# Kernel tuning notes

Hardware: AMD Instinct MI355X
Metric: run time of the kernel (lower is better)

The kernel has to match this reference:

```python
import jax, jax.numpy as jnp
import numpy as np
from jax import lax

B, T, S_ENC = 64, 32, 64
E, H, V = 1024, 1024, 32000


def setup_inputs() -> dict:
    key = jax.random.key(0)
    ks = jax.random.split(key, 12)
    s = 0.02
    return {
        "inputs": jax.random.randint(ks[0], (B, T), 0, V),
        "encoder_outputs": jax.random.normal(ks[1], (B, S_ENC, 2 * H), jnp.float32),
        "h0": jax.random.normal(ks[2], (B, H), jnp.float32) * 0.1,
        "c0": jax.random.normal(ks[3], (B, H), jnp.float32) * 0.1,
        "emb": jax.random.normal(ks[4], (V, E), jnp.float32) * s,
        "W_ih": jax.random.normal(ks[5], (4 * H, E), jnp.float32) * s,
        "W_hh": jax.random.normal(ks[6], (4 * H, H), jnp.float32) * s,
        "b_ih": jnp.zeros((4 * H,), jnp.float32),
        "b_hh": jnp.zeros((4 * H,), jnp.float32),
        "attn_W": jax.random.normal(ks[7], (2 * H, H), jnp.float32) * s,  # Linear(H -> 2H, no bias)
        "comb_W": jax.random.normal(ks[8], (H, 3 * H), jnp.float32) * s,  # Linear(3H -> H)
        "comb_b": jnp.zeros((H,), jnp.float32),
        "out_W": jax.random.normal(ks[9], (V, H), jnp.float32) * s,       # Linear(H -> V)
        "out_b": jnp.zeros((V,), jnp.float32),
    }


def _decode(inputs, encoder_outputs, h0, c0, emb, W_ih, W_hh, b_ih, b_hh,
            attn_W, comb_W, comb_b, out_W, out_b):
    x = emb[inputs]                      # [B, T, E]
    bias = b_ih + b_hh

    def step(carry, x_t):
        h, c = carry                     # [B, H] each
        gates = x_t @ W_ih.T + h @ W_hh.T + bias    # [B, 4H]
        i, f, g, o = jnp.split(gates, 4, axis=-1)   # PyTorch LSTM gate order
        i, f, o = jax.nn.sigmoid(i), jax.nn.sigmoid(f), jax.nn.sigmoid(o)
        c = f * c + i * jnp.tanh(g)
        h = o * jnp.tanh(c)
        # Luong-style attention (faithful to source, incl. softmax over dim=1 of size 1)
        ah = h @ attn_W.T                                        # [B, 2H]
        scores = jnp.einsum('bd,bsd->bs', ah, encoder_outputs)[:, None, :]  # [B,1,S]
        w = jax.nn.softmax(scores, axis=1)                       # size-1 axis -> all ones
        ctx = jnp.einsum('bqs,bsd->bqd', w, encoder_outputs)[:, 0]          # [B, 2H]
        merged = jnp.concatenate([h, ctx], axis=-1)              # [B, 3H]
        out = jnp.tanh(merged @ comb_W.T + comb_b)               # [B, H]
        return (h, c), out

    (h, c), outs = lax.scan(step, (h0, c0), x.transpose(1, 0, 2))
    outputs = outs.transpose(1, 0, 2)                            # [B, T, H]
    logits = outputs @ out_W.T + out_b                           # [B, T, V]
    return logits, h, c


def reference(inputs, encoder_outputs, h0, c0, emb, W_ih, W_hh, b_ih, b_hh,
              attn_W, comb_W, comb_b, out_W, out_b):
    return _decode(inputs, encoder_outputs, h0, c0, emb, W_ih, W_hh, b_ih, b_hh,
                   attn_W, comb_W, comb_b, out_W, out_b)
```

## Files before the change

### kernel.cpp

```cpp
#include <hip/hip_runtime.h>
#include <hip/hip_bf16.h>


typedef unsigned short u16;
typedef unsigned int u32;
typedef short s8v __attribute__((ext_vector_type(8)));
typedef float f4v __attribute__((ext_vector_type(4)));

__device__ __forceinline__ u16 f2bf(float f) {
  unsigned x = __float_as_uint(f);
  return (u16)((x + 0x7fffu + ((x >> 16) & 1u)) >> 16);
}
__device__ __forceinline__ float bf2f(u16 u) {
  return __uint_as_float(((unsigned)u) << 16);
}

__device__ __forceinline__ void gl_lds16(const void* g, void* l) {
  __builtin_amdgcn_global_load_lds(
      (const __attribute__((address_space(1))) u32*)g,
      (__attribute__((address_space(3))) u32*)l, 16, 0, 0);
}

__device__ __forceinline__ int xcd_swz(int bid, int nb) {
  int q8 = nb >> 3, r8 = nb & 7;
  int xcd = bid & 7, idx = bid >> 3;
  return (xcd < r8 ? xcd * (q8 + 1) : r8 * (q8 + 1) + (xcd - r8) * q8) + idx;
}

template <int EPI>
__global__ __launch_bounds__(512, 1) void gemm_p(
    const u16* __restrict__ A, const u16* __restrict__ Bm,
    const float* __restrict__ bias, void* __restrict__ Cp,
    int K, int ldc, int gridM) {
  __shared__ __align__(16) u16 LDS[3 * 24576];

  int swz = xcd_swz((int)blockIdx.x, (int)gridDim.x);
  int mt = swz % gridM, nt = swz / gridM;
  long bm = (long)mt * 128, bn = (long)nt * 256;

  int tid = threadIdx.x;
  int w = tid >> 6, l = tid & 63;
  int wm = w & 1, wn = w >> 1;
  int lr = l & 15, lg = l >> 4;

  int nt_k = K >> 6;

  auto stage = [&](int s, int kt_idx) {
    int kt = kt_idx << 6;
    u16* sa = &LDS[s * 24576];
    u16* sb = &LDS[s * 24576 + 8192];
#pragma unroll
    for (int ch = 0; ch < 2; ++ch) {
      int cb = ch * 512 + w * 64;
      int c = cb + l;
      int row = c >> 3, sp = c & 7;
      gl_lds16(A + (bm + row) * (long)K + kt + ((sp ^ (row & 7)) << 3),
               sa + cb * 8);
    }
#pragma unroll
    for (int ch = 0; ch < 4; ++ch) {
      int cb = ch * 512 + w * 64;
      int c = cb + l;
      int row = c >> 3, sp = c & 7;
      gl_lds16(Bm + (bn + row) * (long)K + kt + ((sp ^ (row & 7)) << 3),
               sb + cb * 8);
    }
  };

  f4v acc[4][4];
#pragma unroll
  for (int i = 0; i < 4; ++i)
#pragma unroll
    for (int j = 0; j < 4; ++j) acc[i][j] = (f4v){0.f, 0.f, 0.f, 0.f};

  stage(0, 0);
  stage(1, 1);
  asm volatile("s_waitcnt vmcnt(6)" ::: "memory");
  __builtin_amdgcn_s_barrier();
  __builtin_amdgcn_sched_barrier(0);

  for (int t = 0; t < nt_k; ++t) {
    if (t + 2 < nt_k) stage((t + 2) % 3, t + 2);
    const u16* sa = &LDS[(t % 3) * 24576];
    const u16* sb = &LDS[(t % 3) * 24576 + 8192];
#pragma unroll
    for (int ks = 0; ks < 2; ++ks) {
      s8v av[4], bv[4];
#pragma unroll
      for (int i = 0; i < 4; ++i) {
        int ra = wm * 64 + i * 16 + lr;
        int pa = (ks * 4 + lg) ^ (ra & 7);
        av[i] = *(const s8v*)((const char*)sa + ra * 128 + pa * 16);
        int rb = wn * 64 + i * 16 + lr;
        int pb = (ks * 4 + lg) ^ (rb & 7);
        bv[i] = *(const s8v*)((const char*)sb + rb * 128 + pb * 16);
      }
      __builtin_amdgcn_s_setprio(1);
#pragma unroll
      for (int mi = 0; mi < 4; ++mi)
#pragma unroll
        for (int ni = 0; ni < 4; ++ni)
          acc[mi][ni] = __builtin_amdgcn_mfma_f32_16x16x32_bf16(
              av[mi], bv[ni], acc[mi][ni], 0, 0, 0);
      __builtin_amdgcn_s_setprio(0);
    }
    if (t + 1 >= nt_k) break;
    if (t + 2 < nt_k) {
      asm volatile("s_waitcnt vmcnt(6)" ::: "memory");
    } else {
      asm volatile("s_waitcnt vmcnt(0)" ::: "memory");
    }
    __builtin_amdgcn_s_barrier();
    __builtin_amdgcn_sched_barrier(0);
  }

#pragma unroll
  for (int mi = 0; mi < 4; ++mi) {
#pragma unroll
    for (int q = 0; q < 4; ++q) {
      long row = bm + wm * 64 + mi * 16 + lg * 4 + q;
#pragma unroll
      for (int ni = 0; ni < 4; ++ni) {
        long col = bn + wn * 64 + ni * 16 + lr;
        float v = acc[mi][ni][q] + bias[col];
        if (EPI == 3)
          ((float*)Cp)[row * (long)ldc + col] = v;
        else
          ((u16*)Cp)[row * (long)ldc + col] = f2bf(v);
      }
    }
  }
}

template <int EPI>
__global__ __launch_bounds__(256, 2) void gemm_bt2(
    const u16* __restrict__ A, const u16* __restrict__ Bm,
    const float* __restrict__ bias, void* __restrict__ Cp,
    int K, int ldc, int gridM) {
  __shared__ __align__(16) u16 As[128 * 64];
  __shared__ __align__(16) u16 Bs[128 * 64];

  int swz = xcd_swz((int)blockIdx.x, (int)gridDim.x);
  int mt = swz % gridM, nt = swz / gridM;
  long bm = (long)mt * 128, bn = (long)nt * 128;

  int tid = threadIdx.x;
  int w = tid >> 6, l = tid & 63;
  int wm = (w & 1) * 64, wn = (w >> 1) * 64;
  int lr = l & 15, lg = l >> 4;

  f4v acc[4][4];
#pragma unroll
  for (int i = 0; i < 4; ++i)
#pragma unroll
    for (int j = 0; j < 4; ++j) acc[i][j] = (f4v){0.f, 0.f, 0.f, 0.f};

  for (int kt = 0; kt < K; kt += 64) {
#pragma unroll
    for (int p = 0; p < 4; ++p) {
      int cb = (p * 4 + w) * 64;
      int c = cb + l;
      int row = c >> 3, ce = (c & 7) * 8;
      gl_lds16(A + (bm + row) * (long)K + kt + ce, &As[cb * 8]);
      gl_lds16(Bm + (bn + row) * (long)K + kt + ce, &Bs[cb * 8]);
    }
    __syncthreads();
#pragma unroll
    for (int ks = 0; ks < 2; ++ks) {
      int kb = ks * 64 + lg * 16;
      s8v av[4], bv[4];
#pragma unroll
      for (int i = 0; i < 4; ++i) {
        av[i] = *(const s8v*)((const char*)&As[0] + (wm + i * 16 + lr) * 128 + kb);
        bv[i] = *(const s8v*)((const char*)&Bs[0] + (wn + i * 16 + lr) * 128 + kb);
      }
#pragma unroll
      for (int mi = 0; mi < 4; ++mi)
#pragma unroll
        for (int ni = 0; ni < 4; ++ni)
          acc[mi][ni] = __builtin_amdgcn_mfma_f32_16x16x32_bf16(
              av[mi], bv[ni], acc[mi][ni], 0, 0, 0);
    }
    __syncthreads();
  }
#pragma unroll
  for (int mi = 0; mi < 4; ++mi) {
#pragma unroll
    for (int q = 0; q < 4; ++q) {
      long row = bm + wm + mi * 16 + lg * 4 + q;
#pragma unroll
      for (int ni = 0; ni < 4; ++ni) {
        long col = bn + wn + ni * 16 + lr;
        float v = acc[mi][ni][q] + bias[col];
        if (EPI == 2) v = tanhf(v);
        if (EPI == 3)
          ((float*)Cp)[row * (long)ldc + col] = v;
        else
          ((u16*)Cp)[row * (long)ldc + col] = f2bf(v);
      }
    }
  }
}

template <int EPI>
__global__ __launch_bounds__(256, 2) void gemm_btf(
    const u16* __restrict__ A, const float* __restrict__ Bm,
    const float* __restrict__ bias, void* __restrict__ Cp,
    int K, int ldc, int gridM) {
  __shared__ __align__(16) u16 As[128][72];
  __shared__ __align__(16) u16 Bs[128][72];
  int swz = xcd_swz((int)blockIdx.x, (int)gridDim.x);
  int mt = swz % gridM, nt = swz / gridM;
  long bm = (long)mt * 128, bn = (long)nt * 128;
  int tid = threadIdx.x;
  int w = tid >> 6, l = tid & 63;
  int wm = (w & 1) * 64, wn = (w >> 1) * 64;
  int lr = l & 15, lg = l >> 4;
  f4v acc[4][4];
#pragma unroll
  for (int i = 0; i < 4; ++i)
#pragma unroll
    for (int j = 0; j < 4; ++j) acc[i][j] = (f4v){0.f, 0.f, 0.f, 0.f};
  for (int kt = 0; kt < K; kt += 64) {
#pragma unroll
    for (int p = 0; p < 4; ++p) {
      int ch = p * 256 + tid;
      int row = ch >> 3, cc = ch & 7;
      *(uint4*)((char*)(&As[0][0]) + row * 144 + cc * 16) =
          *(const uint4*)(A + (bm + row) * (long)K + kt + cc * 8);
      const float* bp = Bm + (bn + row) * (long)K + kt + cc * 8;
      float4 b0 = *(const float4*)bp;
      float4 b1 = *(const float4*)(bp + 4);
      union { u16 t8[8]; uint4 v; } cv;
      cv.t8[0] = f2bf(b0.x); cv.t8[1] = f2bf(b0.y);
      cv.t8[2] = f2bf(b0.z); cv.t8[3] = f2bf(b0.w);
      cv.t8[4] = f2bf(b1.x); cv.t8[5] = f2bf(b1.y);
      cv.t8[6] = f2bf(b1.z); cv.t8[7] = f2bf(b1.w);
      *(uint4*)((char*)(&Bs[0][0]) + row * 144 + cc * 16) = cv.v;
    }
    __syncthreads();
#pragma unroll
    for (int ks = 0; ks < 2; ++ks) {
      int kb = ks * 64 + lg * 16;
      s8v av[4], bv[4];
#pragma unroll
      for (int i = 0; i < 4; ++i) {
        av[i] = *(const s8v*)((const char*)(&As[0][0]) + (wm + i * 16 + lr) * 144 + kb);
        bv[i] = *(const s8v*)((const char*)(&Bs[0][0]) + (wn + i * 16 + lr) * 144 + kb);
      }
#pragma unroll
      for (int mi = 0; mi < 4; ++mi)
#pragma unroll
        for (int ni = 0; ni < 4; ++ni)
          acc[mi][ni] = __builtin_amdgcn_mfma_f32_16x16x32_bf16(
              av[mi], bv[ni], acc[mi][ni], 0, 0, 0);
    }
    __syncthreads();
  }
#pragma unroll
  for (int mi = 0; mi < 4; ++mi) {
#pragma unroll
    for (int q = 0; q < 4; ++q) {
      long row = bm + wm + mi * 16 + lg * 4 + q;
#pragma unroll
      for (int ni = 0; ni < 4; ++ni) {
        long col = bn + wn + ni * 16 + lr;
        float v = acc[mi][ni][q] + bias[col];
        if (EPI == 2) v = tanhf(v);
        if (EPI == 3)
          ((float*)Cp)[row * (long)ldc + col] = v;
        else
          ((u16*)Cp)[row * (long)ldc + col] = f2bf(v);
      }
    }
  }
}

__global__ __launch_bounds__(256, 1) void lstm_step3(
    const u16* __restrict__ Whh, const u16* __restrict__ xproj,
    const u16* __restrict__ h_in, u16* __restrict__ h_next,
    float* __restrict__ c_buf, u16* __restrict__ a2,
    float* __restrict__ hf, float* __restrict__ cf, int t) {
  __shared__ __align__(16) u16 Hs[32 * 1024];
  __shared__ __align__(16) u16 Ws[32 * 1024];
  __shared__ float Gs[32][33];

  int bid = blockIdx.x;
  int j = bid & 127, bh = bid >> 7;
  int colbase = j * 8;
  int tid = threadIdx.x, w = tid >> 6, l = tid & 63;
  int bq = w & 1, nh = w >> 1;
  int lr = l & 15, lg = l >> 4;

  int hi = tid >> 7;
  int ps = tid & 127;
#pragma unroll
  for (int p = 0; p < 16; ++p) {
    int r = 2 * p + hi;
    int sl = ps ^ (r & 7);
    gl_lds16(h_in + (bh * 32 + r) * 1024 + sl * 8, &Hs[(p * 4 + w) * 512]);
    int g = r >> 3, rr = r & 7;
    gl_lds16(Whh + (long)(g * 1024 + colbase + rr) * 1024 + sl * 8,
             &Ws[(p * 4 + w) * 512]);
  }
  __syncthreads();

  int ar = bq * 16 + lr;
  int br = nh * 16 + lr;
  int axor = (ar & 7), bxor = (br & 7);
  f4v acc0 = {0.f, 0.f, 0.f, 0.f}, acc1 = {0.f, 0.f, 0.f, 0.f};
#pragma unroll
  for (int kc = 0; kc < 32; kc += 2) {
    {
      int s = kc * 4 + lg;
      s8v av = *(const s8v*)((const char*)Hs + ar * 2048 + (s ^ axor) * 16);
      s8v bv = *(const s8v*)((const char*)Ws + br * 2048 + (s ^ bxor) * 16);
      acc0 = __builtin_amdgcn_mfma_f32_16x16x32_bf16(av, bv, acc0, 0, 0, 0);
    }
    {
      int s = (kc + 1) * 4 + lg;
      s8v av = *(const s8v*)((const char*)Hs + ar * 2048 + (s ^ axor) * 16);
      s8v bv = *(const s8v*)((const char*)Ws + br * 2048 + (s ^ bxor) * 16);
      acc1 = __builtin_amdgcn_mfma_f32_16x16x32_bf16(av, bv, acc1, 0, 0, 0);
    }
  }
#pragma unroll
  for (int q = 0; q < 4; ++q)
    Gs[bq * 16 + lg * 4 + q][nh * 16 + lr] = acc0[q] + acc1[q];
  __syncthreads();

  int b = tid >> 3, rr = tid & 7;
  int gb = bh * 32 + b;
  int col = colbase + rr;
  const u16* xp = xproj + (long)(gb * 32 + t) * 4096;
  float pi = Gs[b][rr]      + bf2f(xp[col]);
  float pf = Gs[b][8 + rr]  + bf2f(xp[1024 + col]);
  float pg = Gs[b][16 + rr] + bf2f(xp[2048 + col]);
  float po = Gs[b][24 + rr] + bf2f(xp[3072 + col]);
  float iv = 1.f / (1.f + expf(-pi));
  float fv = 1.f / (1.f + expf(-pf));
  float ov = 1.f / (1.f + expf(-po));
  float gv = tanhf(pg);
  float co = c_buf[gb * 1024 + col];
  float cn = fv * co + iv * gv;
  float hn = ov * tanhf(cn);
  c_buf[gb * 1024 + col] = cn;
  u16 hb = f2bf(hn);
  h_next[gb * 1024 + col] = hb;
  a2[(long)(gb * 32 + t) * 3072 + col] = hb;
  if (t == 31) {
    hf[gb * 1024 + col] = hn;
    cf[gb * 1024 + col] = cn;
  }
}

__global__ void k_misc(const float* __restrict__ bih, const float* __restrict__ bhh,
                       const float* __restrict__ h0, const float* __restrict__ c0,
                       float* __restrict__ bias, u16* __restrict__ hbuf0,
                       float* __restrict__ cbuf) {
  int i = blockIdx.x * 256 + threadIdx.x;
  if (i < 4096) bias[i] = bih[i] + bhh[i];
  if (i < 65536) {
    hbuf0[i] = f2bf(h0[i]);
    cbuf[i] = c0[i];
  }
}

__global__ void k_cvt8(const float* __restrict__ src, u16* __restrict__ dst, int n8) {
  int i = blockIdx.x * 256 + threadIdx.x;
  if (i >= n8) return;
  const float4* s = (const float4*)(src + (long)i * 8);
  float4 a = s[0], b = s[1];
  union { u16 t[8]; uint4 v; } cv;
  cv.t[0] = f2bf(a.x); cv.t[1] = f2bf(a.y); cv.t[2] = f2bf(a.z); cv.t[3] = f2bf(a.w);
  cv.t[4] = f2bf(b.x); cv.t[5] = f2bf(b.y); cv.t[6] = f2bf(b.z); cv.t[7] = f2bf(b.w);
  ((uint4*)dst)[i] = cv.v;
}

__global__ void k_emb8(const int* __restrict__ inp, const float* __restrict__ emb,
                       u16* __restrict__ dst) {
  int i = blockIdx.x * 256 + threadIdx.x;
  int r = i >> 7, k8 = (i & 127) * 8;
  const float* s = emb + (long)inp[r] * 1024 + k8;
  float4 a = *(const float4*)s, b = *(const float4*)(s + 4);
  union { u16 t[8]; uint4 v; } cv;
  cv.t[0] = f2bf(a.x); cv.t[1] = f2bf(a.y); cv.t[2] = f2bf(a.z); cv.t[3] = f2bf(a.w);
  cv.t[4] = f2bf(b.x); cv.t[5] = f2bf(b.y); cv.t[6] = f2bf(b.z); cv.t[7] = f2bf(b.w);
  ((uint4*)dst)[i] = cv.v;
}

__global__ void k_ctx2(const float* __restrict__ enc, u16* __restrict__ a2) {
  int b = blockIdx.x;
  int dg = threadIdx.x;
  float s[8] = {0.f, 0.f, 0.f, 0.f, 0.f, 0.f, 0.f, 0.f};
  for (int si = 0; si < 64; ++si) {
    const float* p = enc + ((long)(b * 64 + si)) * 2048 + dg * 8;
    float4 x = *(const float4*)p, y = *(const float4*)(p + 4);
    s[0] += x.x; s[1] += x.y; s[2] += x.z; s[3] += x.w;
    s[4] += y.x; s[5] += y.y; s[6] += y.z; s[7] += y.w;
  }
  union { u16 t[8]; uint4 v; } cv;
#pragma unroll
  for (int e = 0; e < 8; ++e) cv.t[e] = f2bf(s[e]);
  for (int t = 0; t < 32; ++t)
    *(uint4*)(a2 + (long)(b * 32 + t) * 3072 + 1024 + dg * 8) = cv.v;
}

extern "C" void kernel_launch(void* const* d_in, const int* in_sizes, int n_in,
                              void* d_out, int out_size, void* d_ws, size_t ws_size,
                              hipStream_t stream) {
  (void)in_sizes; (void)n_in; (void)out_size;
  const int*   inputs = (const int*)d_in[0];
  const float* enc    = (const float*)d_in[1];
  const float* h0     = (const float*)d_in[2];
  const float* c0     = (const float*)d_in[3];
  const float* emb    = (const float*)d_in[4];
  const float* Wih    = (const float*)d_in[5];
  const float* Whh    = (const float*)d_in[6];
  const float* bih    = (const float*)d_in[7];
  const float* bhh    = (const float*)d_in[8];
  const float* combW  = (const float*)d_in[10];
  const float* combb  = (const float*)d_in[11];
  const float* outW   = (const float*)d_in[12];
  const float* outb   = (const float*)d_in[13];
  float* out = (float*)d_out;

  char* ws = (char*)d_ws;
  size_t off = 0;
  auto alloc = [&](size_t bytes) {
    char* p = ws + off;
    off += (bytes + 255) & ~(size_t)255;
    return p;
  };
  u16*   WHH_BF = (u16*)  alloc(4096ull * 1024 * 2);
  u16*   XPROJ  = (u16*)  alloc(2048ull * 4096 * 2);
  u16*   EMBX   = (u16*)  alloc(2048ull * 1024 * 2);
  u16*   A2     = (u16*)  alloc(2048ull * 3072 * 2);
  u16*   OUTS   = (u16*)  alloc(2048ull * 1024 * 2);
  float* BIAS   = (float*)alloc(4096 * 4);
  u16*   HBUF   = (u16*)  alloc(2ull * 65536 * 2);
  float* CBUF   = (float*)alloc(65536 * 4);
  u16*   WIH_BF   = (u16*)alloc(4096ull * 1024 * 2);
  u16*   COMBW_BF = (u16*)alloc(1024ull * 3072 * 2);
  size_t off_w1 = off;
  u16*   OUTW_BF  = (u16*)alloc(32000ull * 1024 * 2);
  size_t off_w2 = off;
  bool haveW1 = ws_size >= off_w1;
  bool haveW2 = ws_size >= off_w2;

  k_misc<<<dim3(256), dim3(256), 0, stream>>>(bih, bhh, h0, c0, BIAS, HBUF, CBUF);
  k_cvt8<<<dim3(2048), dim3(256), 0, stream>>>(Whh, WHH_BF, 524288);
  k_emb8<<<dim3(1024), dim3(256), 0, stream>>>(inputs, emb, EMBX);
  k_ctx2<<<dim3(64), dim3(256), 0, stream>>>(enc, A2);
  if (haveW1) {
    k_cvt8<<<dim3(2048), dim3(256), 0, stream>>>(Wih, WIH_BF, 524288);
    k_cvt8<<<dim3(1536), dim3(256), 0, stream>>>(combW, COMBW_BF, 393216);
  }
  if (haveW2)
    k_cvt8<<<dim3(16000), dim3(256), 0, stream>>>(outW, OUTW_BF, 4096000);

  if (haveW1)
    gemm_p<1><<<dim3(256), dim3(512), 0, stream>>>(EMBX, WIH_BF, BIAS, XPROJ,
                                                   1024, 4096, 16);
  else
    gemm_btf<1><<<dim3(512), dim3(256), 0, stream>>>(EMBX, Wih, BIAS, XPROJ,
                                                     1024, 4096, 16);

  for (int t = 0; t < 32; ++t) {
    u16* hin  = HBUF + (t & 1) * 65536;
    u16* hout = HBUF + ((t + 1) & 1) * 65536;
    lstm_step3<<<dim3(256), dim3(256), 0, stream>>>(
        WHH_BF, XPROJ, hin, hout, CBUF, A2,
        out + 65536000, out + 65536000 + 65536, t);
  }

  if (haveW1)
    gemm_bt2<2><<<dim3(128), dim3(256), 0, stream>>>(A2, COMBW_BF, combb, OUTS,
                                                     3072, 1024, 16);
  else
    gemm_btf<2><<<dim3(128), dim3(256), 0, stream>>>(A2, combW, combb, OUTS,
                                                     3072, 1024, 16);
  if (haveW2)
    gemm_p<3><<<dim3(2000), dim3(512), 0, stream>>>(OUTS, OUTW_BF, outb, d_out,
                                                    1024, 32000, 16);
  else
    gemm_btf<3><<<dim3(4000), dim3(256), 0, stream>>>(OUTS, outW, outb, d_out,
                                                      1024, 32000, 16);
}
```

Before: 599.3 us.

## Use 256x256 tiled GEMM for output projection with double-buffered LDS

Adds a new GEMM kernel that uses 256x256 output tiles instead of 128x256, with a two-stage LDS double buffer and an XOR-swizzled layout. The final vocabulary projection now runs on it with half as many blocks. Larger tiles raise arithmetic intensity and cut redundant loads of the B matrix (the out weights). In exchange the kernel holds more accumulator registers per thread and has one fewer pipeline stage than the previous three-stage kernel, which may expose memory latency.

```diff
diff --git a/kernel.cpp b/kernel.cpp
--- a/kernel.cpp
+++ b/kernel.cpp
@@ -25,6 +25,102 @@
   int q8 = nb >> 3, r8 = nb & 7;
   int xcd = bid & 7, idx = bid >> 3;
   return (xcd < r8 ? xcd * (q8 + 1) : r8 * (q8 + 1) + (xcd - r8) * q8) + idx;
+}
+
+template <int EPI>
+__global__ __launch_bounds__(512, 1) void gemm_q(
+    const u16* __restrict__ A, const u16* __restrict__ Bm,
+    const float* __restrict__ bias, void* __restrict__ Cp,
+    int K, int ldc, int gridM) {
+  __shared__ __align__(16) u16 LDS[2 * 32768];
+
+  int swz = xcd_swz((int)blockIdx.x, (int)gridDim.x);
+  int mt = swz % gridM, nt = swz / gridM;
+  long bm = (long)mt * 256, bn = (long)nt * 256;
+
+  int tid = threadIdx.x;
+  int w = tid >> 6, l = tid & 63;
+  int wm = w & 1, wn = w >> 1;
+  int lr = l & 15, lg = l >> 4;
+
+  int nt_k = K >> 6;
+
+  auto stage = [&](int s, int kt_idx) {
+    int kt = kt_idx << 6;
+    u16* sa = &LDS[s * 32768];
+    u16* sb = &LDS[s * 32768 + 16384];
+#pragma unroll
+    for (int ch = 0; ch < 4; ++ch) {
+      int cb = ch * 512 + w * 64;
+      int c = cb + l;
+      int row = c >> 3, sp = c & 7;
+      int ko = kt + ((sp ^ (row & 7)) << 3);
+      gl_lds16(A + (bm + row) * (long)K + ko, sa + cb * 8);
+      gl_lds16(Bm + (bn + row) * (long)K + ko, sb + cb * 8);
+    }
+  };
+
+  f4v acc[8][4];
+#pragma unroll
+  for (int i = 0; i < 8; ++i)
+#pragma unroll
+    for (int j = 0; j < 4; ++j) acc[i][j] = (f4v){0.f, 0.f, 0.f, 0.f};
+
+  stage(0, 0);
+  asm volatile("s_waitcnt vmcnt(0)" ::: "memory");
+  __builtin_amdgcn_s_barrier();
+  __builtin_amdgcn_sched_barrier(0);
+
+  for (int t = 0; t < nt_k; ++t) {
+    if (t + 1 < nt_k) stage((t + 1) & 1, t + 1);
+    const u16* sa = &LDS[(t & 1) * 32768];
+    const u16* sb = &LDS[(t & 1) * 32768 + 16384];
+#pragma unroll
+    for (int ks = 0; ks < 2; ++ks) {
+      s8v av[8], bv[4];
+#pragma unroll
+      for (int i = 0; i < 8; ++i) {
+        int ra = wm * 128 + i * 16 + lr;
+        int pa = (ks * 4 + lg) ^ (ra & 7);
+        av[i] = *(const s8v*)((const char*)sa + ra * 128 + pa * 16);
+      }
+#pragma unroll
+      for (int i = 0; i < 4; ++i) {
+        int rb = wn * 64 + i * 16 + lr;
+        int pb = (ks * 4 + lg) ^ (rb & 7);
+        bv[i] = *(const s8v*)((const char*)sb + rb * 128 + pb * 16);
+      }
+      __builtin_amdgcn_s_setprio(1);
+#pragma unroll
+      for (int mi = 0; mi < 8; ++mi)
+#pragma unroll
+        for (int ni = 0; ni < 4; ++ni)
+          acc[mi][ni] = __builtin_amdgcn_mfma_f32_16x16x32_bf16(
+              av[mi], bv[ni], acc[mi][ni], 0, 0, 0);
+      __builtin_amdgcn_s_setprio(0);
+    }
+    if (t + 1 >= nt_k) break;
+    asm volatile("s_waitcnt vmcnt(0)" ::: "memory");
+    __builtin_amdgcn_s_barrier();
+    __builtin_amdgcn_sched_barrier(0);
+  }
+
+#pragma unroll
+  for (int mi = 0; mi < 8; ++mi) {
+#pragma unroll
+    for (int q = 0; q < 4; ++q) {
+      long row = bm + wm * 128 + mi * 16 + lg * 4 + q;
+#pragma unroll
+      for (int ni = 0; ni < 4; ++ni) {
+        long col = bn + wn * 64 + ni * 16 + lr;
+        float v = acc[mi][ni][q] + bias[col];
+        if (EPI == 3)
+          ((float*)Cp)[row * (long)ldc + col] = v;
+        else
+          ((u16*)Cp)[row * (long)ldc + col] = f2bf(v);
+      }
+    }
+  }
 }
 
 template <int EPI>
@@ -481,8 +577,8 @@
     gemm_btf<2><<<dim3(128), dim3(256), 0, stream>>>(A2, combW, combb, OUTS,
                                                      3072, 1024, 16);
   if (haveW2)
-    gemm_p<3><<<dim3(2000), dim3(512), 0, stream>>>(OUTS, OUTW_BF, outb, d_out,
-                                                    1024, 32000, 16);
+    gemm_q<3><<<dim3(1000), dim3(512), 0, stream>>>(OUTS, OUTW_BF, outb, d_out,
+                                                    1024, 32000, 8);
   else
     gemm_btf<3><<<dim3(4000), dim3(256), 0, stream>>>(OUTS, outW, outb, d_out,
                                                       1024, 32000, 16);
```

Result: faster. 578.5 us (-3.5%).
